# Kernel optimization log

Measured on AMD Instinct MI355X. Metric: run time of the kernel, lower is better.

Reference implementation:

```python
import jax, jax.numpy as jnp
import numpy as np

N_NODES = 100000
N_EDGES = 1600000
HIDDEN = 128
N_FILTERS = 64
CUTOFF = 8.0
BN_EPS = 1e-3  # keras BatchNormalization default epsilon


def setup_inputs() -> dict:
    key = jax.random.key(0)
    ks = jax.random.split(key, 12)
    x = jax.random.normal(ks[0], (N_NODES, HIDDEN), dtype=jnp.float32)
    edge_index = jax.random.randint(ks[1], (2, N_EDGES), 0, N_NODES, dtype=jnp.int32)
    edge_weight = jax.random.uniform(ks[2], (N_EDGES,), dtype=jnp.float32) * CUTOFF
    edge_attr = jax.random.uniform(ks[3], (N_EDGES, 1), dtype=jnp.float32)
    s = 0.05
    # filter_net: Dense(1->64, tanh), Dense(64->64)
    Wf1 = jax.random.normal(ks[4], (1, N_FILTERS), dtype=jnp.float32) * s
    bf1 = jnp.zeros((N_FILTERS,), jnp.float32)
    Wf2 = jax.random.normal(ks[5], (N_FILTERS, N_FILTERS), dtype=jnp.float32) * s
    bf2 = jnp.zeros((N_FILTERS,), jnp.float32)
    # interaction_net: Dense(128->128, softplus), Dense(128->128)
    Wi1 = jax.random.normal(ks[6], (HIDDEN, HIDDEN), dtype=jnp.float32) * s
    bi1 = jnp.zeros((HIDDEN,), jnp.float32)
    Wi2 = jax.random.normal(ks[7], (HIDDEN, HIDDEN), dtype=jnp.float32) * s
    bi2 = jnp.zeros((HIDDEN,), jnp.float32)
    # BatchNormalization (inference: moving stats)
    gamma = jnp.ones((HIDDEN,), jnp.float32)
    beta = jnp.zeros((HIDDEN,), jnp.float32)
    mov_mean = jax.random.normal(ks[8], (HIDDEN,), dtype=jnp.float32) * 0.01
    mov_var = jnp.ones((HIDDEN,), jnp.float32)
    return {"x": x, "edge_index": edge_index, "edge_weight": edge_weight,
            "edge_attr": edge_attr, "Wf1": Wf1, "bf1": bf1, "Wf2": Wf2, "bf2": bf2,
            "Wi1": Wi1, "bi1": bi1, "Wi2": Wi2, "bi2": bi2,
            "gamma": gamma, "beta": beta, "mov_mean": mov_mean, "mov_var": mov_var}


def reference(x, edge_index, edge_weight, edge_attr, Wf1, bf1, Wf2, bf2,
              Wi1, bi1, Wi2, bi2, gamma, beta, mov_mean, mov_var):
    row, col = edge_index[0], edge_index[1]
    # continuous filters with smooth cosine cutoff
    scaled = edge_weight * (2.0 / CUTOFF) - 1.0                    # [E]
    h = jnp.tanh(scaled[:, None] @ Wf1 + bf1)                      # [E, F]
    filters = h @ Wf2 + bf2                                        # [E, F]
    cut = 0.5 * (jnp.cos(edge_weight * jnp.pi / CUTOFF) + 1.0)
    cut = jnp.where(edge_weight <= CUTOFF, cut, 0.0)               # [E]
    filters = filters * cut[:, None]
    # Original: (neighbor[:, None, :] * filters[:, :, None]).sum(axis=1)
    # == neighbor * filters.sum(-1, keepdims) — same math, no [E,F,H] tensor.
    fsum = jnp.sum(filters, axis=-1, keepdims=True)                # [E, 1]
    messages = x[col] * fsum                                       # [E, H]
    agg = jax.ops.segment_sum(messages, row, num_segments=x.shape[0])  # [N, H]
    out = jax.nn.softplus(agg @ Wi1 + bi1) @ Wi2 + bi2             # [N, H]
    # BatchNormalization, inference mode (training=False)
    out = gamma * (out - mov_mean) * jax.lax.rsqrt(mov_var + BN_EPS) + beta
    return out
```

## Files before the change

kernel.cpp:

```cpp
#include <hip/hip_runtime.h>
#include <math.h>

#define HIDDEN 128
#define NFILT 64
#define SCAN_B 1024
#define LUTK 2048

typedef __attribute__((ext_vector_type(8))) short bf16x8;
typedef __attribute__((ext_vector_type(4))) float f32x4;
typedef __attribute__((ext_vector_type(4))) float f32x4v;
typedef __attribute__((ext_vector_type(2))) int i32x2;

__device__ __forceinline__ short f2bf(float f) {
    unsigned u = __float_as_uint(f);
    unsigned r = (u + 0x7fffu + ((u >> 16) & 1u)) >> 16;
    return (short)r;
}
__device__ __forceinline__ float bf2f(unsigned short u) {
    return __uint_as_float(((unsigned)u) << 16);
}

__device__ __forceinline__ float softplus_fast(float v) {
    float e = __builtin_amdgcn_exp2f(v * 1.4426950408889634f);
    float r = 0.69314718055994531f * __builtin_amdgcn_logf(1.0f + e);
    return (v > 80.f) ? v : r;
}

__global__ void wsum_kernel(const float* __restrict__ Wf2, const float* __restrict__ bf2,
                            float* __restrict__ wsum, float* __restrict__ bsum) {
    int j = threadIdx.x;
    float s = 0.f;
    for (int f = 0; f < NFILT; ++f) s += Wf2[j * NFILT + f];
    wsum[j] = s;
    if (j == 0) {
        float b = 0.f;
        for (int f = 0; f < NFILT; ++f) b += bf2[f];
        *bsum = b;
    }
}

__device__ __forceinline__ float edge_coeff(float w,
                                            const float* sW, const float* sB,
                                            const float* sS, float bsum) {
    float s = fmaf(w, 0.25f, -1.0f);
    float acc = bsum;
    #pragma unroll 8
    for (int j = 0; j < NFILT; ++j)
        acc += tanhf(fmaf(s, sW[j], sB[j])) * sS[j];
    float cut = (w <= 8.0f) ? 0.5f * (cosf(w * 0.39269908169872414f) + 1.0f) : 0.0f;
    return acc * cut;
}

__global__ void lut_kernel(const float* __restrict__ Wf1, const float* __restrict__ bf1,
                           const float* __restrict__ wsum, const float* __restrict__ bsum,
                           float* __restrict__ lut) {
    int i = blockIdx.x * 256 + threadIdx.x;
    if (i > LUTK) return;
    float w = 8.0f * (float)i / (float)LUTK;
    lut[i] = edge_coeff(w, Wf1, bf1, wsum, *bsum);
}

__device__ __forceinline__ float lut_eval(const float* sl, float w) {
    float t = w * ((float)LUTK / 8.0f);
    t = fminf(fmaxf(t, 0.f), (float)LUTK);
    int i = (int)t;
    i = min(i, LUTK - 1);
    return fmaf(t - (float)i, sl[i + 1] - sl[i], sl[i]);
}

__global__ void prep_w_kernel(const float* __restrict__ Wi1, const float* __restrict__ Wi2,
                              short* __restrict__ W1T, short* __restrict__ W2T,
                              const float* __restrict__ Wf2, const float* __restrict__ bf2,
                              float* __restrict__ wsum, float* __restrict__ bsum,
                              const float* __restrict__ bi2,
                              const float* __restrict__ gamma, const float* __restrict__ beta,
                              const float* __restrict__ mean, const float* __restrict__ var,
                              float* __restrict__ scf, float* __restrict__ shf) {
    int idx = blockIdx.x * 256 + threadIdx.x;
    const float* src = (idx < 16384) ? Wi1 : Wi2;
    short* dst = (idx < 16384) ? W1T : W2T;
    int i = idx & 16383;
    int k = i >> 7, n = i & 127;
    dst[n * HIDDEN + k] = f2bf(src[i]);

    if (blockIdx.x == 0 && threadIdx.x < 64) {
        int j = threadIdx.x;
        float s = 0.f;
        for (int f = 0; f < NFILT; ++f) s += Wf2[j * NFILT + f];
        wsum[j] = s;
        if (j == 0) {
            float b = 0.f;
            for (int f = 0; f < NFILT; ++f) b += bf2[f];
            *bsum = b;
        }
    }
    if (blockIdx.x == 1 && threadIdx.x < HIDDEN) {
        int j = threadIdx.x;
        float sc = gamma[j] * rsqrtf(var[j] + 1e-3f);
        scf[j] = sc;
        shf[j] = (bi2[j] - mean[j]) * sc + beta[j];
    }
}

__global__ __launch_bounds__(256) void x2q_count_kernel(
    const float* __restrict__ x, signed char* __restrict__ xq,
    float* __restrict__ xscale, int N16,
    const int* __restrict__ rows, int* __restrict__ deg,
    int* __restrict__ rank, int E) {
    int i = blockIdx.x * 256 + threadIdx.x;
    if (i < E) rank[i] = atomicAdd(&deg[__builtin_nontemporal_load(&rows[i])], 1);
    if (i < N16) {
        int node = i >> 4, lane = i & 15;
        const float* xp = &x[(size_t)node * HIDDEN + lane * 8];
        const f32x4v v0 = __builtin_nontemporal_load((const f32x4v*)xp);
        const f32x4v v1 = __builtin_nontemporal_load((const f32x4v*)(xp + 4));
        float v[8] = {v0[0], v0[1], v0[2], v0[3], v1[0], v1[1], v1[2], v1[3]};
        float m = 0.f;
        #pragma unroll
        for (int j = 0; j < 8; ++j) m = fmaxf(m, fabsf(v[j]));
        #pragma unroll
        for (int off = 8; off > 0; off >>= 1)
            m = fmaxf(m, __shfl_xor(m, off, 16));
        float si = (m > 0.f) ? 127.f / m : 0.f;
        int q[8];
        #pragma unroll
        for (int j = 0; j < 8; ++j) q[j] = __float2int_rn(v[j] * si);
        int lo = (q[0] & 0xff) | ((q[1] & 0xff) << 8) |
                 ((q[2] & 0xff) << 16) | ((q[3] & 0xff) << 24);
        int hi = (q[4] & 0xff) | ((q[5] & 0xff) << 8) |
                 ((q[6] & 0xff) << 16) | ((q[7] & 0xff) << 24);
        *(int2*)&xq[(size_t)node * HIDDEN + lane * 8] = make_int2(lo, hi);
        if (lane == 0) xscale[node] = m * (1.f / 127.f);
    }
}

__global__ void count_rank_kernel(const int* __restrict__ rows, int* __restrict__ deg,
                                  int* __restrict__ rank, int E) {
    int e = blockIdx.x * blockDim.x + threadIdx.x;
    if (e < E) rank[e] = atomicAdd(&deg[rows[e]], 1);
}

__global__ void count_kernel(const int* __restrict__ rows, int* __restrict__ deg, int E) {
    int e = blockIdx.x * blockDim.x + threadIdx.x;
    if (e < E) atomicAdd(&deg[rows[e]], 1);
}

__global__ __launch_bounds__(SCAN_B) void scan_p1(const int* __restrict__ deg,
                                                  int* __restrict__ bsums, int N) {
    __shared__ int red[SCAN_B];
    int i = blockIdx.x * SCAN_B + threadIdx.x;
    red[threadIdx.x] = (i < N) ? deg[i] : 0;
    __syncthreads();
    for (int off = SCAN_B / 2; off > 0; off >>= 1) {
        if (threadIdx.x < off) red[threadIdx.x] += red[threadIdx.x + off];
        __syncthreads();
    }
    if (threadIdx.x == 0) bsums[blockIdx.x] = red[0];
}

__global__ __launch_bounds__(SCAN_B) void scan_p2(int* __restrict__ bsums, int B) {
    __shared__ int part[SCAN_B];
    int t = threadIdx.x;
    part[t] = (t < B) ? bsums[t] : 0;
    __syncthreads();
    for (int off = 1; off < SCAN_B; off <<= 1) {
        int v = (t >= off) ? part[t - off] : 0;
        __syncthreads();
        part[t] += v;
        __syncthreads();
    }
    if (t < B) bsums[t] = (t == 0) ? 0 : part[t - 1];
}

template <bool WRITE_CURSOR>
__global__ __launch_bounds__(SCAN_B) void scan_p3_t(int* __restrict__ deg,
                                                    const int* __restrict__ bsums,
                                                    int* __restrict__ offs, int N) {
    __shared__ int part[SCAN_B];
    int t = threadIdx.x;
    int i = blockIdx.x * SCAN_B + t;
    int d = (i < N) ? deg[i] : 0;
    part[t] = d;
    __syncthreads();
    for (int off = 1; off < SCAN_B; off <<= 1) {
        int v = (t >= off) ? part[t - off] : 0;
        __syncthreads();
        part[t] += v;
        __syncthreads();
    }
    int pre = bsums[blockIdx.x] + part[t] - d;
    if (i < N) {
        offs[i] = pre;
        if (WRITE_CURSOR) deg[i] = pre;
        if (i == N - 1) offs[N] = pre + d;
    }
}

__global__ __launch_bounds__(256) void fill_rank_q_kernel(
    const int* __restrict__ rows, const int* __restrict__ cols,
    const float* __restrict__ ew, const int* __restrict__ rank,
    const int* __restrict__ offs, const float* __restrict__ xscale,
    const float* __restrict__ lut, int2* __restrict__ epack, int E) {
    __shared__ float sl[LUTK + 1];
    for (int i = threadIdx.x; i <= LUTK; i += 256) sl[i] = lut[i];
    __syncthreads();
    int e = blockIdx.x * 256 + threadIdx.x;
    if (e >= E) return;
    float f = lut_eval(sl, __builtin_nontemporal_load(&ew[e]));
    int r = __builtin_nontemporal_load(&rows[e]);
    int c = __builtin_nontemporal_load(&cols[e]);
    float fs = f * xscale[c];
    int pos = offs[r] + __builtin_nontemporal_load(&rank[e]);
    epack[pos] = make_int2(c, __float_as_int(fs));
}

__global__ __launch_bounds__(256) void fill_rank_kernel(
    const int* __restrict__ rows, const int* __restrict__ cols,
    const float* __restrict__ ew, const int* __restrict__ rank,
    const int* __restrict__ offs, const float* __restrict__ lut,
    int2* __restrict__ epack, int E) {
    __shared__ float sl[LUTK + 1];
    for (int i = threadIdx.x; i <= LUTK; i += 256) sl[i] = lut[i];
    __syncthreads();
    int e = blockIdx.x * 256 + threadIdx.x;
    if (e >= E) return;
    float f = lut_eval(sl, __builtin_nontemporal_load(&ew[e]));
    int pos = offs[__builtin_nontemporal_load(&rows[e])] +
              __builtin_nontemporal_load(&rank[e]);
    epack[pos] = make_int2(__builtin_nontemporal_load(&cols[e]), __float_as_int(f));
}

__global__ __launch_bounds__(256) void fill_cursor_kernel(
    const int* __restrict__ rows, const int* __restrict__ cols,
    const float* __restrict__ ew, int* __restrict__ cursor,
    const float* __restrict__ lut, int2* __restrict__ epack, int E) {
    __shared__ float sl[LUTK + 1];
    for (int i = threadIdx.x; i <= LUTK; i += 256) sl[i] = lut[i];
    __syncthreads();
    int e = blockIdx.x * 256 + threadIdx.x;
    if (e >= E) return;
    float f = lut_eval(sl, ew[e]);
    int pos = atomicAdd(&cursor[rows[e]], 1);
    epack[pos] = make_int2(cols[e], __float_as_int(f));
}

__device__ __forceinline__ void qfma8(int lo, int hi, float f, float* a) {
    a[0] = fmaf((float)((int)(((unsigned)lo) << 24) >> 24), f, a[0]);
    a[1] = fmaf((float)((int)(((unsigned)lo) << 16) >> 24), f, a[1]);
    a[2] = fmaf((float)((int)(((unsigned)lo) << 8) >> 24), f, a[2]);
    a[3] = fmaf((float)(lo >> 24), f, a[3]);
    a[4] = fmaf((float)((int)(((unsigned)hi) << 24) >> 24), f, a[4]);
    a[5] = fmaf((float)((int)(((unsigned)hi) << 16) >> 24), f, a[5]);
    a[6] = fmaf((float)((int)(((unsigned)hi) << 8) >> 24), f, a[6]);
    a[7] = fmaf((float)(hi >> 24), f, a[7]);
}

__global__ __launch_bounds__(256) void gather_q8_kernel(const int* __restrict__ offs,
                                                        const int2* __restrict__ epack,
                                                        const signed char* __restrict__ xq,
                                                        short* __restrict__ aggh, int N) {
    int t = threadIdx.x;
    int node = blockIdx.x * 16 + (t >> 4);
    if (node >= N) return;
    int lane = t & 15;
    int s = offs[node], eend = offs[node + 1];
    const signed char* xb = xq + lane * 8;

    float a[8];
    #pragma unroll
    for (int j = 0; j < 8; ++j) a[j] = 0.f;

    int i = s;
    for (; i + 4 <= eend; i += 4) {
        i32x2 p0 = __builtin_nontemporal_load((const i32x2*)&epack[i]);
        i32x2 p1 = __builtin_nontemporal_load((const i32x2*)&epack[i + 1]);
        i32x2 p2 = __builtin_nontemporal_load((const i32x2*)&epack[i + 2]);
        i32x2 p3 = __builtin_nontemporal_load((const i32x2*)&epack[i + 3]);
        int2 q0 = *(const int2*)(xb + (size_t)p0[0] * HIDDEN);
        int2 q1 = *(const int2*)(xb + (size_t)p1[0] * HIDDEN);
        int2 q2 = *(const int2*)(xb + (size_t)p2[0] * HIDDEN);
        int2 q3 = *(const int2*)(xb + (size_t)p3[0] * HIDDEN);
        qfma8(q0.x, q0.y, __int_as_float(p0[1]), a);
        qfma8(q1.x, q1.y, __int_as_float(p1[1]), a);
        qfma8(q2.x, q2.y, __int_as_float(p2[1]), a);
        qfma8(q3.x, q3.y, __int_as_float(p3[1]), a);
    }
    for (; i < eend; ++i) {
        i32x2 p = __builtin_nontemporal_load((const i32x2*)&epack[i]);
        int2 q = *(const int2*)(xb + (size_t)p[0] * HIDDEN);
        qfma8(q.x, q.y, __int_as_float(p[1]), a);
    }

    bf16x8 o;
    #pragma unroll
    for (int j = 0; j < 8; ++j) o[j] = f2bf(a[j]);
    *(bf16x8*)&aggh[(size_t)node * HIDDEN + lane * 8] = o;
}

__global__ __launch_bounds__(256) void gather_kernel(const int* __restrict__ offs,
                                                     const int2* __restrict__ epack,
                                                     const float* __restrict__ x,
                                                     float* __restrict__ agg, int N) {
    int t = threadIdx.x;
    int node = blockIdx.x * 8 + (t >> 5);
    if (node >= N) return;
    int lane = t & 31;
    int s = offs[node], eend = offs[node + 1];
    float4 acc = make_float4(0.f, 0.f, 0.f, 0.f);
    int i = s;
    for (; i + 2 <= eend; i += 2) {
        int2 p0 = epack[i];
        int2 p1 = epack[i + 1];
        float4 x0 = *(const float4*)&x[(size_t)p0.x * HIDDEN + lane * 4];
        float4 x1 = *(const float4*)&x[(size_t)p1.x * HIDDEN + lane * 4];
        float f0 = __int_as_float(p0.y), f1 = __int_as_float(p1.y);
        acc.x = fmaf(x0.x, f0, acc.x); acc.y = fmaf(x0.y, f0, acc.y);
        acc.z = fmaf(x0.z, f0, acc.z); acc.w = fmaf(x0.w, f0, acc.w);
        acc.x = fmaf(x1.x, f1, acc.x); acc.y = fmaf(x1.y, f1, acc.y);
        acc.z = fmaf(x1.z, f1, acc.z); acc.w = fmaf(x1.w, f1, acc.w);
    }
    for (; i < eend; ++i) {
        int2 p = epack[i];
        float f = __int_as_float(p.y);
        const float4 xv = *(const float4*)&x[(size_t)p.x * HIDDEN + lane * 4];
        acc.x = fmaf(xv.x, f, acc.x);
        acc.y = fmaf(xv.y, f, acc.y);
        acc.z = fmaf(xv.z, f, acc.z);
        acc.w = fmaf(xv.w, f, acc.w);
    }
    *(float4*)&agg[(size_t)node * HIDDEN + lane * 4] = acc;
}

#define HROW 136

#define WSWZ(b) ((b) ^ ((((b) >> 8) & 7) << 4))

__global__ __launch_bounds__(512) void mlp_mfma_bf_kernel(
    const short* __restrict__ aggh, float* __restrict__ io,
    const short* __restrict__ W1T, const short* __restrict__ W2T,
    const float* __restrict__ bi1,
    const float* __restrict__ scf, const float* __restrict__ shf,
    int N) {
    __shared__ short wS[HIDDEN * HIDDEN];
    __shared__ short hS[128 * HROW];

    const int t = threadIdx.x;
    const int wave = t >> 6;
    const int lane = t & 63;
    const int quad = lane >> 4;
    const int m16  = lane & 15;
    const int row0 = blockIdx.x * 128 + wave * 16;
    const int arow = row0 + m16;

    const int swzmask = (m16 & 7) << 4;

    bf16x8 w2r[4];
    {
        const bf16x8* w1v = (const bf16x8*)W1T;
        const bf16x8* w2v = (const bf16x8*)W2T;
        bf16x8 w1r[4];
        #pragma unroll
        for (int j = 0; j < 4; ++j) w1r[j] = w1v[t + 512 * j];
        #pragma unroll
        for (int j = 0; j < 4; ++j) w2r[j] = w2v[t + 512 * j];
        #pragma unroll
        for (int j = 0; j < 4; ++j) {
            int b = (t + 512 * j) * 16;
            *(bf16x8*)((char*)wS + WSWZ(b)) = w1r[j];
        }
    }

    float b1v[8];
    #pragma unroll
    for (int ct = 0; ct < 8; ++ct) b1v[ct] = bi1[ct * 16 + m16];

    f32x4 acc[8];
    #pragma unroll
    for (int ct = 0; ct < 8; ++ct) acc[ct] = (f32x4)(0.f);

    __syncthreads();

    #pragma unroll
    for (int ks = 0; ks < 4; ++ks) {
        bf16x8 a;
        if (arow < N) {
            a = *(const bf16x8*)&aggh[(size_t)arow * HIDDEN + ks * 32 + quad * 8];
        } else {
            #pragma unroll
            for (int j = 0; j < 8; ++j) a[j] = 0;
        }
        const char* bbase = (const char*)wS + m16 * 256 + ((ks * 64 + quad * 16) ^ swzmask);
        #pragma unroll
        for (int ct = 0; ct < 8; ++ct) {
            bf16x8 b = *(const bf16x8*)(bbase + ct * 4096);
            acc[ct] = __builtin_amdgcn_mfma_f32_16x16x32_bf16(a, b, acc[ct], 0, 0, 0);
        }
    }

    #pragma unroll
    for (int ct = 0; ct < 8; ++ct) {
        int col = ct * 16 + m16;
        #pragma unroll
        for (int r = 0; r < 4; ++r) {
            int lrow = wave * 16 + quad * 4 + r;
            float h = softplus_fast(acc[ct][r] + b1v[ct]);
            hS[lrow * HROW + col] = f2bf(h);
        }
        acc[ct] = (f32x4)(0.f);
    }
    __syncthreads();

    #pragma unroll
    for (int j = 0; j < 4; ++j) {
        int b = (t + 512 * j) * 16;
        *(bf16x8*)((char*)wS + WSWZ(b)) = w2r[j];
    }
    __syncthreads();

    float scv[8], shv[8];
    #pragma unroll
    for (int ct = 0; ct < 8; ++ct) {
        scv[ct] = scf[ct * 16 + m16];
        shv[ct] = shf[ct * 16 + m16];
    }

    #pragma unroll
    for (int ks = 0; ks < 4; ++ks) {
        bf16x8 a = *(const bf16x8*)&hS[(wave * 16 + m16) * HROW + ks * 32 + quad * 8];
        const char* bbase = (const char*)wS + m16 * 256 + ((ks * 64 + quad * 16) ^ swzmask);
        #pragma unroll
        for (int ct = 0; ct < 8; ++ct) {
            bf16x8 b = *(const bf16x8*)(bbase + ct * 4096);
            acc[ct] = __builtin_amdgcn_mfma_f32_16x16x32_bf16(a, b, acc[ct], 0, 0, 0);
        }
    }

    #pragma unroll
    for (int r = 0; r < 4; ++r) {
        int grow = row0 + quad * 4 + r;
        if (grow < N) {
            float* p = &io[(size_t)grow * HIDDEN + m16];
            #pragma unroll
            for (int ct = 0; ct < 8; ++ct)
                __builtin_nontemporal_store(fmaf(acc[ct][r], scv[ct], shv[ct]), p + ct * 16);
        }
    }
}

__global__ __launch_bounds__(256) void mlp_mfma_kernel(
    float* io,
    const short* __restrict__ W1T, const short* __restrict__ W2T,
    const float* __restrict__ bi1,
    const float* __restrict__ scf, const float* __restrict__ shf,
    int N) {
    __shared__ short hS[64 * HROW];

    const int t = threadIdx.x;
    const int wave = t >> 6;
    const int lane = t & 63;
    const int quad = lane >> 4;
    const int m16  = lane & 15;
    const int row0 = blockIdx.x * 64 + wave * 16;
    const int arow = row0 + m16;

    f32x4 acc[8];
    #pragma unroll
    for (int ct = 0; ct < 8; ++ct) acc[ct] = (f32x4)(0.f);

    #pragma unroll
    for (int ks = 0; ks < 4; ++ks) {
        bf16x8 a;
        if (arow < N) {
            const float* ap = &io[(size_t)arow * HIDDEN + ks * 32 + quad * 8];
            float4 v0 = *(const float4*)ap;
            float4 v1 = *(const float4*)(ap + 4);
            a[0] = f2bf(v0.x); a[1] = f2bf(v0.y); a[2] = f2bf(v0.z); a[3] = f2bf(v0.w);
            a[4] = f2bf(v1.x); a[5] = f2bf(v1.y); a[6] = f2bf(v1.z); a[7] = f2bf(v1.w);
        } else {
            #pragma unroll
            for (int j = 0; j < 8; ++j) a[j] = 0;
        }
        #pragma unroll
        for (int ct = 0; ct < 8; ++ct) {
            bf16x8 b = *(const bf16x8*)&W1T[(ct * 16 + m16) * HIDDEN + ks * 32 + quad * 8];
            acc[ct] = __builtin_amdgcn_mfma_f32_16x16x32_bf16(a, b, acc[ct], 0, 0, 0);
        }
    }

    #pragma unroll
    for (int ct = 0; ct < 8; ++ct) {
        int col = ct * 16 + m16;
        float b1 = bi1[col];
        #pragma unroll
        for (int r = 0; r < 4; ++r) {
            int lrow = wave * 16 + quad * 4 + r;
            float h = softplus_fast(acc[ct][r] + b1);
            hS[lrow * HROW + col] = f2bf(h);
            acc[ct][r] = 0.f;
        }
    }
    __syncthreads();

    #pragma unroll
    for (int ks = 0; ks < 4; ++ks) {
        bf16x8 a = *(const bf16x8*)&hS[(wave * 16 + m16) * HROW + ks * 32 + quad * 8];
        #pragma unroll
        for (int ct = 0; ct < 8; ++ct) {
            bf16x8 b = *(const bf16x8*)&W2T[(ct * 16 + m16) * HIDDEN + ks * 32 + quad * 8];
            acc[ct] = __builtin_amdgcn_mfma_f32_16x16x32_bf16(a, b, acc[ct], 0, 0, 0);
        }
    }

    #pragma unroll
    for (int ct = 0; ct < 8; ++ct) {
        int col = ct * 16 + m16;
        float sc = scf[col], sh = shf[col];
        #pragma unroll
        for (int r = 0; r < 4; ++r) {
            int grow = row0 + quad * 4 + r;
            if (grow < N)
                io[(size_t)grow * HIDDEN + col] = fmaf(acc[ct][r], sc, sh);
        }
    }
}

__global__ void edge_filter_kernel(const float* __restrict__ ew,
                                   const float* __restrict__ Wf1, const float* __restrict__ bf1,
                                   const float* __restrict__ wsum, const float* __restrict__ bsum,
                                   float* __restrict__ fs, int E) {
    __shared__ float sW[NFILT], sB[NFILT], sS[NFILT];
    if (threadIdx.x < NFILT) {
        sW[threadIdx.x] = Wf1[threadIdx.x];
        sB[threadIdx.x] = bf1[threadIdx.x];
        sS[threadIdx.x] = wsum[threadIdx.x];
    }
    __syncthreads();
    int e = blockIdx.x * blockDim.x + threadIdx.x;
    if (e >= E) return;
    fs[e] = edge_coeff(ew[e], sW, sB, sS, *bsum);
}

__global__ void scatter_kernel(const int* __restrict__ rows, const int* __restrict__ cols,
                               const float* __restrict__ x, const float* __restrict__ fs,
                               float* __restrict__ agg, int E) {
    int t = threadIdx.x;
    int e = blockIdx.x * 8 + (t >> 5);
    if (e >= E) return;
    int lane = t & 31;
    int r = rows[e];
    int c = cols[e];
    float f = fs[e];
    const float4 xv = *(const float4*)&x[c * HIDDEN + lane * 4];
    float* dst = &agg[r * HIDDEN + lane * 4];
    atomicAdd(dst + 0, xv.x * f);
    atomicAdd(dst + 1, xv.y * f);
    atomicAdd(dst + 2, xv.z * f);
    atomicAdd(dst + 3, xv.w * f);
}

__global__ __launch_bounds__(256) void mlp_kernel(
    float* __restrict__ io,
    const float* __restrict__ Wi1, const float* __restrict__ bi1,
    const float* __restrict__ Wi2, const float* __restrict__ bi2,
    const float* __restrict__ gamma, const float* __restrict__ beta,
    const float* __restrict__ mean, const float* __restrict__ var,
    int N) {
    __shared__ float As[64 * HIDDEN];
    __shared__ float Wh[64 * HIDDEN];

    const int t = threadIdx.x;
    const int row0 = blockIdx.x * 64;
    const int col4 = (t & 31) * 4;
    const int rgrp = t >> 5;

    #pragma unroll
    for (int i = 0; i < 8; ++i) {
        int f4 = t + 256 * i;
        int r = f4 >> 5, c4 = (f4 & 31) * 4;
        int node = row0 + r;
        float4 v = make_float4(0.f, 0.f, 0.f, 0.f);
        if (node < N) v = *(const float4*)&io[node * HIDDEN + c4];
        *(float4*)&As[r * HIDDEN + c4] = v;
    }

    float acc[8][4];
    #pragma unroll
    for (int r = 0; r < 8; ++r)
        for (int j = 0; j < 4; ++j) acc[r][j] = 0.f;

    for (int kh = 0; kh < 2; ++kh) {
        __syncthreads();
        #pragma unroll
        for (int i = 0; i < 8; ++i) {
            int f4 = t + 256 * i;
            int kr = f4 >> 5, c4 = (f4 & 31) * 4;
            *(float4*)&Wh[kr * HIDDEN + c4] = *(const float4*)&Wi1[(kh * 64 + kr) * HIDDEN + c4];
        }
        __syncthreads();
        for (int k = 0; k < 64; ++k) {
            float4 w = *(const float4*)&Wh[k * HIDDEN + col4];
            #pragma unroll
            for (int r = 0; r < 8; ++r) {
                float a = As[(rgrp + 8 * r) * HIDDEN + kh * 64 + k];
                acc[r][0] = fmaf(a, w.x, acc[r][0]);
                acc[r][1] = fmaf(a, w.y, acc[r][1]);
                acc[r][2] = fmaf(a, w.z, acc[r][2]);
                acc[r][3] = fmaf(a, w.w, acc[r][3]);
            }
        }
    }
    __syncthreads();

    {
        float4 b = *(const float4*)&bi1[col4];
        float bv[4] = {b.x, b.y, b.z, b.w};
        #pragma unroll
        for (int r = 0; r < 8; ++r) {
            float hv[4];
            #pragma unroll
            for (int j = 0; j < 4; ++j) {
                float v = acc[r][j] + bv[j];
                hv[j] = softplus_fast(v);
                acc[r][j] = 0.f;
            }
            *(float4*)&As[(rgrp + 8 * r) * HIDDEN + col4] =
                make_float4(hv[0], hv[1], hv[2], hv[3]);
        }
    }

    for (int kh = 0; kh < 2; ++kh) {
        __syncthreads();
        #pragma unroll
        for (int i = 0; i < 8; ++i) {
            int f4 = t + 256 * i;
            int kr = f4 >> 5, c4 = (f4 & 31) * 4;
            *(float4*)&Wh[kr * HIDDEN + c4] = *(const float4*)&Wi2[(kh * 64 + kr) * HIDDEN + c4];
        }
        __syncthreads();
        for (int k = 0; k < 64; ++k) {
            float4 w = *(const float4*)&Wh[k * HIDDEN + col4];
            #pragma unroll
            for (int r = 0; r < 8; ++r) {
                float a = As[(rgrp + 8 * r) * HIDDEN + kh * 64 + k];
                acc[r][0] = fmaf(a, w.x, acc[r][0]);
                acc[r][1] = fmaf(a, w.y, acc[r][1]);
                acc[r][2] = fmaf(a, w.z, acc[r][2]);
                acc[r][3] = fmaf(a, w.w, acc[r][3]);
            }
        }
    }

    {
        float4 b2 = *(const float4*)&bi2[col4];
        float4 g  = *(const float4*)&gamma[col4];
        float4 be = *(const float4*)&beta[col4];
        float4 mu = *(const float4*)&mean[col4];
        float4 va = *(const float4*)&var[col4];
        float bv[4]  = {b2.x, b2.y, b2.z, b2.w};
        float gv[4]  = {g.x, g.y, g.z, g.w};
        float bev[4] = {be.x, be.y, be.z, be.w};
        float muv[4] = {mu.x, mu.y, mu.z, mu.w};
        float vav[4] = {va.x, va.y, va.z, va.w};
        float sc[4];
        #pragma unroll
        for (int j = 0; j < 4; ++j) sc[j] = gv[j] * rsqrtf(vav[j] + 1e-3f);
        #pragma unroll
        for (int r = 0; r < 8; ++r) {
            int node = row0 + rgrp + 8 * r;
            if (node < N) {
                float o[4];
                #pragma unroll
                for (int j = 0; j < 4; ++j)
                    o[j] = (acc[r][j] + bv[j] - muv[j]) * sc[j] + bev[j];
                *(float4*)&io[node * HIDDEN + col4] = make_float4(o[0], o[1], o[2], o[3]);
            }
        }
    }
}

extern "C" void kernel_launch(void* const* d_in, const int* in_sizes, int n_in,
                              void* d_out, int out_size, void* d_ws, size_t ws_size,
                              hipStream_t stream) {
    const float* x    = (const float*)d_in[0];
    const int*   ei   = (const int*)d_in[1];
    const float* ew   = (const float*)d_in[2];
    const float* Wf1  = (const float*)d_in[4];
    const float* bf1  = (const float*)d_in[5];
    const float* Wf2  = (const float*)d_in[6];
    const float* bf2  = (const float*)d_in[7];
    const float* Wi1  = (const float*)d_in[8];
    const float* bi1  = (const float*)d_in[9];
    const float* Wi2  = (const float*)d_in[10];
    const float* bi2  = (const float*)d_in[11];
    const float* gam  = (const float*)d_in[12];
    const float* bet  = (const float*)d_in[13];
    const float* mmu  = (const float*)d_in[14];
    const float* mva  = (const float*)d_in[15];

    const int N = in_sizes[0] / HIDDEN;
    const int E = in_sizes[2];
    const int* rows = ei;
    const int* cols = ei + E;

    float* io = (float*)d_out;

    const int B = (N + SCAN_B - 1) / SCAN_B;

    char* ws = (char*)d_ws;
    int*   deg    = (int*)ws;
    int*   offs   = deg + N;
    int*   bsums  = offs + N + 1;
    float* wsumv  = (float*)(bsums + B);
    float* bsumv  = wsumv + NFILT;
    float* lut    = bsumv + 1;
    size_t hdr_ints  = (size_t)(2 * N + 1 + B + NFILT + 1 + LUTK + 1);
    size_t epack_off = ((hdr_ints * 4) + 15) & ~(size_t)15;
    int2*  epack  = (int2*)(ws + epack_off);
    size_t wT_off = (epack_off + (size_t)E * sizeof(int2) + 15) & ~(size_t)15;
    short* W1T    = (short*)(ws + wT_off);
    short* W2T    = W1T + HIDDEN * HIDDEN;
    float* scf    = (float*)(W2T + HIDDEN * HIDDEN);
    float* shf    = scf + HIDDEN;
    size_t base_need = wT_off + 2 * HIDDEN * HIDDEN * sizeof(short) + 2 * HIDDEN * sizeof(float);
    size_t rank_off  = (base_need + 15) & ~(size_t)15;
    int*   rank   = (int*)(ws + rank_off);
    size_t rank_need = rank_off + (size_t)E * sizeof(int);
    size_t xq_off    = (rank_need + 15) & ~(size_t)15;
    signed char* xq  = (signed char*)(ws + xq_off);
    size_t xs_off    = (xq_off + (size_t)N * HIDDEN + 15) & ~(size_t)15;
    float* xscale    = (float*)(ws + xs_off);
    size_t ag_off    = (xs_off + (size_t)N * sizeof(float) + 15) & ~(size_t)15;
    short* aggh      = (short*)(ws + ag_off);
    size_t bf_need   = ag_off + (size_t)N * HIDDEN * sizeof(short);

    if (ws_size >= base_need && B <= SCAN_B) {
        const bool use_rank = (ws_size >= rank_need);
        const bool use_bf   = (ws_size >= bf_need);
        hipMemsetAsync(deg, 0, (size_t)N * sizeof(int), stream);
        prep_w_kernel<<<128, 256, 0, stream>>>(Wi1, Wi2, W1T, W2T,
                                               Wf2, bf2, wsumv, bsumv,
                                               bi2, gam, bet, mmu, mva, scf, shf);
        lut_kernel<<<(LUTK + 256) / 256, 256, 0, stream>>>(Wf1, bf1, wsumv, bsumv, lut);
        if (use_bf) {
            int N16 = N * 16;
            int work = (N16 > E) ? N16 : E;
            x2q_count_kernel<<<(work + 255) / 256, 256, 0, stream>>>(x, xq, xscale, N16,
                                                                     rows, deg, rank, E);
        } else if (use_rank) {
            count_rank_kernel<<<(E + 255) / 256, 256, 0, stream>>>(rows, deg, rank, E);
        } else {
            count_kernel<<<(E + 255) / 256, 256, 0, stream>>>(rows, deg, E);
        }
        scan_p1<<<B, SCAN_B, 0, stream>>>(deg, bsums, N);
        scan_p2<<<1, SCAN_B, 0, stream>>>(bsums, B);
        if (use_bf) {
            scan_p3_t<false><<<B, SCAN_B, 0, stream>>>(deg, bsums, offs, N);
            fill_rank_q_kernel<<<(E + 255) / 256, 256, 0, stream>>>(rows, cols, ew, rank,
                                                                    offs, xscale, lut,
                                                                    epack, E);
            gather_q8_kernel<<<(N + 15) / 16, 256, 0, stream>>>(offs, epack, xq, aggh, N);
            mlp_mfma_bf_kernel<<<(N + 127) / 128, 512, 0, stream>>>(aggh, io, W1T, W2T,
                                                                    bi1, scf, shf, N);
        } else if (use_rank) {
            scan_p3_t<false><<<B, SCAN_B, 0, stream>>>(deg, bsums, offs, N);
            fill_rank_kernel<<<(E + 255) / 256, 256, 0, stream>>>(rows, cols, ew, rank,
                                                                  offs, lut, epack, E);
            gather_kernel<<<(N + 7) / 8, 256, 0, stream>>>(offs, epack, x, io, N);
            mlp_mfma_kernel<<<(N + 63) / 64, 256, 0, stream>>>(io, W1T, W2T, bi1, scf, shf, N);
        } else {
            scan_p3_t<true><<<B, SCAN_B, 0, stream>>>(deg, bsums, offs, N);
            fill_cursor_kernel<<<(E + 255) / 256, 256, 0, stream>>>(rows, cols, ew, deg,
                                                                    lut, epack, E);
            gather_kernel<<<(N + 7) / 8, 256, 0, stream>>>(offs, epack, x, io, N);
            mlp_mfma_kernel<<<(N + 63) / 64, 256, 0, stream>>>(io, W1T, W2T, bi1, scf, shf, N);
        }
    } else {
        float* fs = (float*)d_ws;
        float* w2 = fs + E;
        float* b2 = w2 + NFILT;
        hipMemsetAsync(d_out, 0, (size_t)out_size * sizeof(float), stream);
        wsum_kernel<<<1, 64, 0, stream>>>(Wf2, bf2, w2, b2);
        edge_filter_kernel<<<(E + 255) / 256, 256, 0, stream>>>(ew, Wf1, bf1, w2, b2, fs, E);
        scatter_kernel<<<(E + 7) / 8, 256, 0, stream>>>(rows, cols, x, fs, io, E);
        mlp_kernel<<<(N + 63) / 64, 256, 0, stream>>>(io, Wi1, bi1, Wi2, bi2,
                                                      gam, bet, mmu, mva, N);
    }
}
```

Measured before the change: 343.4 us.

## Privatize degree-count atomics per XCD and merge with a row scan

Degree counting now goes to eight per-XCD copies of the degree array, picked by the hardware XCC id, so each atomic stays within one die's L2 instead of contending across dies. The rank value packs the XCD id with the local rank. A new row-scan kernel turns the per-XCD counts into prefix offsets and a total degree, and the fill kernel adds the matching XCD offset. The cost is an extra kernel, a memset eight times larger, and one more gather load per edge. Workgroup-scope atomics on memory shared by other workgroups on the same XCD are only correct if every workgroup on that die sees the same L2.

Measured after the change: 354.8 us. +3.3%, slower.

```diff
diff --git a/kernel.cpp b/kernel.cpp
--- a/kernel.cpp
+++ b/kernel.cpp
@@ -5,6 +5,7 @@
 #define NFILT 64
 #define SCAN_B 1024
 #define LUTK 2048
+#define NXCD 8
 
 typedef __attribute__((ext_vector_type(8))) short bf16x8;
 typedef __attribute__((ext_vector_type(4))) float f32x4;
@@ -18,6 +19,12 @@
 }
 __device__ __forceinline__ float bf2f(unsigned short u) {
     return __uint_as_float(((unsigned)u) << 16);
+}
+
+__device__ __forceinline__ int xcc_id() {
+    int x;
+    asm volatile("s_getreg_b32 %0, hwreg(HW_REG_XCC_ID)" : "=s"(x));
+    return x & (NXCD - 1);
 }
 
 __device__ __forceinline__ float softplus_fast(float v) {
@@ -105,10 +112,16 @@
 __global__ __launch_bounds__(256) void x2q_count_kernel(
     const float* __restrict__ x, signed char* __restrict__ xq,
     float* __restrict__ xscale, int N16,
-    const int* __restrict__ rows, int* __restrict__ deg,
-    int* __restrict__ rank, int E) {
+    const int* __restrict__ rows, int* __restrict__ deg_x,
+    int* __restrict__ rank, int E, int N) {
     int i = blockIdx.x * 256 + threadIdx.x;
-    if (i < E) rank[i] = atomicAdd(&deg[__builtin_nontemporal_load(&rows[i])], 1);
+    if (i < E) {
+        int r = rows[i];
+        int xcd = xcc_id();
+        int lr = __hip_atomic_fetch_add(&deg_x[(size_t)xcd * N + r], 1,
+                                        __ATOMIC_RELAXED, __HIP_MEMORY_SCOPE_WORKGROUP);
+        rank[i] = (xcd << 24) | lr;
+    }
     if (i < N16) {
         int node = i >> 4, lane = i & 15;
         const float* xp = &x[(size_t)node * HIDDEN + lane * 8];
@@ -132,6 +145,20 @@
         *(int2*)&xq[(size_t)node * HIDDEN + lane * 8] = make_int2(lo, hi);
         if (lane == 0) xscale[node] = m * (1.f / 127.f);
     }
+}
+
+__global__ __launch_bounds__(256) void rowscan8_kernel(int* __restrict__ deg_x,
+                                                       int* __restrict__ deg, int N) {
+    int r = blockIdx.x * 256 + threadIdx.x;
+    if (r >= N) return;
+    int s = 0;
+    #pragma unroll
+    for (int c = 0; c < NXCD; ++c) {
+        int v = deg_x[(size_t)c * N + r];
+        deg_x[(size_t)c * N + r] = s;
+        s += v;
+    }
+    deg[r] = s;
 }
 
 __global__ void count_rank_kernel(const int* __restrict__ rows, int* __restrict__ deg,
@@ -199,8 +226,9 @@
 __global__ __launch_bounds__(256) void fill_rank_q_kernel(
     const int* __restrict__ rows, const int* __restrict__ cols,
     const float* __restrict__ ew, const int* __restrict__ rank,
-    const int* __restrict__ offs, const float* __restrict__ xscale,
-    const float* __restrict__ lut, int2* __restrict__ epack, int E) {
+    const int* __restrict__ offs, const int* __restrict__ deg_x,
+    const float* __restrict__ xscale, const float* __restrict__ lut,
+    int2* __restrict__ epack, int E, int N) {
     __shared__ float sl[LUTK + 1];
     for (int i = threadIdx.x; i <= LUTK; i += 256) sl[i] = lut[i];
     __syncthreads();
@@ -209,8 +237,11 @@
     float f = lut_eval(sl, __builtin_nontemporal_load(&ew[e]));
     int r = __builtin_nontemporal_load(&rows[e]);
     int c = __builtin_nontemporal_load(&cols[e]);
+    int pk = __builtin_nontemporal_load(&rank[e]);
+    int xcd = ((unsigned)pk) >> 24;
+    int lr = pk & 0xffffff;
     float fs = f * xscale[c];
-    int pos = offs[r] + __builtin_nontemporal_load(&rank[e]);
+    int pos = offs[r] + deg_x[(size_t)xcd * N + r] + lr;
     epack[pos] = make_int2(c, __float_as_int(fs));
 }
 
@@ -731,12 +762,17 @@
     float* xscale    = (float*)(ws + xs_off);
     size_t ag_off    = (xs_off + (size_t)N * sizeof(float) + 15) & ~(size_t)15;
     short* aggh      = (short*)(ws + ag_off);
+    int*   deg_x     = (int*)aggh;
     size_t bf_need   = ag_off + (size_t)N * HIDDEN * sizeof(short);
 
     if (ws_size >= base_need && B <= SCAN_B) {
         const bool use_rank = (ws_size >= rank_need);
         const bool use_bf   = (ws_size >= bf_need);
-        hipMemsetAsync(deg, 0, (size_t)N * sizeof(int), stream);
+        if (use_bf) {
+            hipMemsetAsync(deg_x, 0, (size_t)NXCD * N * sizeof(int), stream);
+        } else {
+            hipMemsetAsync(deg, 0, (size_t)N * sizeof(int), stream);
+        }
         prep_w_kernel<<<128, 256, 0, stream>>>(Wi1, Wi2, W1T, W2T,
                                                Wf2, bf2, wsumv, bsumv,
                                                bi2, gam, bet, mmu, mva, scf, shf);
@@ -745,7 +781,9 @@
             int N16 = N * 16;
             int work = (N16 > E) ? N16 : E;
             x2q_count_kernel<<<(work + 255) / 256, 256, 0, stream>>>(x, xq, xscale, N16,
-                                                                     rows, deg, rank, E);
+                                                                     rows, deg_x, rank,
+                                                                     E, N);
+            rowscan8_kernel<<<(N + 255) / 256, 256, 0, stream>>>(deg_x, deg, N);
         } else if (use_rank) {
             count_rank_kernel<<<(E + 255) / 256, 256, 0, stream>>>(rows, deg, rank, E);
         } else {
@@ -756,8 +794,8 @@
         if (use_bf) {
             scan_p3_t<false><<<B, SCAN_B, 0, stream>>>(deg, bsums, offs, N);
             fill_rank_q_kernel<<<(E + 255) / 256, 256, 0, stream>>>(rows, cols, ew, rank,
-                                                                    offs, xscale, lut,
-                                                                    epack, E);
+                                                                    offs, deg_x, xscale,
+                                                                    lut, epack, E, N);
             gather_q8_kernel<<<(N + 15) / 16, 256, 0, stream>>>(offs, epack, xq, aggh, N);
             mlp_mfma_bf_kernel<<<(N + 127) / 128, 512, 0, stream>>>(aggh, io, W1T, W2T,
                                                                     bi1, scf, shf, N);
```
